# Optimization experiments

Measured on AMD Instinct MI355X. Metric: run time of the kernel, lower is better.

The kernel has to match this reference:

```python
import jax, jax.numpy as jnp
import numpy as np

N, E, F, H = 50000, 800000, 64, 4
NEG_SLOPE = 0.2
LN_EPS = 1e-5


def setup_inputs() -> dict:
    key = jax.random.key(0)
    ks = jax.random.split(key, 12)
    h = jax.random.normal(ks[0], (N, F), dtype=jnp.float32)
    src = jax.random.randint(ks[1], (E,), 0, N, dtype=jnp.int32)
    dst = jax.random.randint(ks[2], (E,), 0, N, dtype=jnp.int32)
    s = 1.0 / np.sqrt(F)
    fc_w = jax.random.uniform(ks[3], (F, H * F), jnp.float32, -s, s)
    attn_l = jax.random.normal(ks[4], (H, F), dtype=jnp.float32) * s
    attn_r = jax.random.normal(ks[5], (H, F), dtype=jnp.float32) * s
    gat_bias = jnp.zeros((H * F,), dtype=jnp.float32)
    so = 1.0 / np.sqrt(H * F)
    out_w = jax.random.uniform(ks[6], (H * F, F), jnp.float32, -so, so)
    out_b = jax.random.uniform(ks[7], (F,), jnp.float32, -so, so)
    ln_g = jnp.ones((F,), dtype=jnp.float32)
    ln_b = jnp.zeros((F,), dtype=jnp.float32)
    return {"h": h, "src": src, "dst": dst, "fc_w": fc_w, "attn_l": attn_l,
            "attn_r": attn_r, "gat_bias": gat_bias, "out_w": out_w,
            "out_b": out_b, "ln_g": ln_g, "ln_b": ln_b}


def reference(h, src, dst, fc_w, attn_l, attn_r, gat_bias, out_w, out_b, ln_g, ln_b):
    # --- GATConv (DGL semantics) ---
    feat = (h @ fc_w).reshape(N, H, F)                      # [N,H,F]
    el = jnp.einsum('nhf,hf->nh', feat, attn_l)             # [N,H]
    er = jnp.einsum('nhf,hf->nh', feat, attn_r)             # [N,H]
    e = jax.nn.leaky_relu(el[src] + er[dst], NEG_SLOPE)     # [E,H]
    # edge softmax over incoming edges of each dst node
    m = jax.ops.segment_max(e, dst, num_segments=N)         # [N,H]
    ex = jnp.exp(e - m[dst])                                # [E,H]
    z = jax.ops.segment_sum(ex, dst, num_segments=N)        # [N,H]
    alpha = ex / z[dst]                                     # [E,H]
    msg = feat[src] * alpha[:, :, None]                     # [E,H,F]
    rst = jax.ops.segment_sum(msg, dst, num_segments=N)     # [N,H,F]
    rst = rst + gat_bias.reshape(H, F)
    # --- out linear + layernorm ---
    x = rst.reshape(N, H * F) @ out_w + out_b               # [N,F]
    mu = jnp.mean(x, axis=-1, keepdims=True)
    var = jnp.var(x, axis=-1, keepdims=True)
    return (x - mu) * jax.lax.rsqrt(var + LN_EPS) * ln_g + ln_b
```

## Files before the change

### kernel.cpp

```cpp
#include <hip/hip_runtime.h>

#define NN 50000
#define EE 800000
#define FF 64
#define HH 4
#define HF 256
#define NEG_SLOPE 0.2f
#define LN_EPS 1e-5f
#define WPACK_N (4 * 8 * 64 * 8)
#define NTILE (NN / 16)
#define TROW 264

typedef __attribute__((ext_vector_type(8))) short s8v;
typedef __attribute__((ext_vector_type(4))) float f4v;

__device__ __forceinline__ unsigned short f32_to_bf16_rne(float x) {
  unsigned int u = __float_as_uint(x);
  unsigned int r = u + 0x7FFFu + ((u >> 16) & 1u);
  return (unsigned short)(r >> 16);
}

__device__ __forceinline__ float readlane_f(float v, int l) {
  return __uint_as_float(
      (unsigned)__builtin_amdgcn_readlane((int)__float_as_uint(v), l));
}

__global__ __launch_bounds__(256) void k_prep(
    const float* __restrict__ fc_w, const float* __restrict__ out_w,
    const float* __restrict__ attn_l, const float* __restrict__ attn_r,
    const float* __restrict__ gat_bias, const float* __restrict__ out_b,
    unsigned short* __restrict__ wpack, float* __restrict__ alv,
    float* __restrict__ arv, float* __restrict__ outb2,
    int* __restrict__ cnt) {
  const int idx = blockIdx.x * 256 + threadIdx.x;
  if (idx < WPACK_N) {
    const int j = idx & 7;
    const int l = (idx >> 3) & 63;
    const int t = (idx >> 9) & 7;
    const int ct = idx >> 12;
    const int k = 32 * t + (l >> 4) * 8 + j;
    const int c = 16 * ct + (l & 15);
    const int hh = k >> 6, kk = k & 63;
    const float* fw = fc_w + kk * HF + hh * FF;
    const float* ow = out_w + (size_t)(hh * FF) * FF + c;
    float acc = 0.f;
#pragma unroll
    for (int ff = 0; ff < FF; ++ff) acc = fmaf(fw[ff], ow[(size_t)ff * FF], acc);
    wpack[idx] = f32_to_bf16_rne(acc);
  } else if (idx < WPACK_N + 512) {
    const int i = idx - WPACK_N;
    const int hh = (i >> 6) & 3, kk = i & 63;
    const float* fw = fc_w + kk * HF + hh * FF;
    const float* at = (i < 256 ? attn_l : attn_r) + hh * FF;
    float acc = 0.f;
#pragma unroll
    for (int ff = 0; ff < FF; ++ff) acc = fmaf(fw[ff], at[ff], acc);
    (i < 256 ? alv : arv)[(hh << 6) | kk] = acc;
  } else if (idx < WPACK_N + 512 + FF) {
    const int c = idx - WPACK_N - 512;
    float acc = out_b[c];
    for (int k = 0; k < HF; ++k) acc = fmaf(gat_bias[k], out_w[(size_t)k * FF + c], acc);
    outb2[c] = acc;
  }
  if (idx < NN) cnt[idx] = 0;
}

__global__ __launch_bounds__(256) void k_elr(
    const float* __restrict__ h, const float* __restrict__ alv,
    const float* __restrict__ arv, unsigned short* __restrict__ hb,
    float* __restrict__ el, float* __restrict__ er) {
  const int wave = threadIdx.x >> 6;
  const int lane = threadIdx.x & 63;
  const int n0 = blockIdx.x * 16 + wave * 4;
  float av[4], bv[4];
#pragma unroll
  for (int hh = 0; hh < 4; ++hh) {
    av[hh] = alv[(hh << 6) | lane];
    bv[hh] = arv[(hh << 6) | lane];
  }
#pragma unroll
  for (int r = 0; r < 4; ++r) {
    const int n = n0 + r;
    const float hv = h[(size_t)n * FF + lane];
    hb[(size_t)n * FF + lane] = f32_to_bf16_rne(hv);
    float p[8];
#pragma unroll
    for (int hh = 0; hh < 4; ++hh) { p[hh] = hv * av[hh]; p[4 + hh] = hv * bv[hh]; }
#pragma unroll
    for (int off = 1; off < 64; off <<= 1) {
#pragma unroll
      for (int q = 0; q < 8; ++q) p[q] += __shfl_xor(p[q], off, 64);
    }
    if (lane == 0) {
      *(float4*)(el + (size_t)n * 4) = make_float4(p[0], p[1], p[2], p[3]);
      *(float4*)(er + (size_t)n * 4) = make_float4(p[4], p[5], p[6], p[7]);
    }
  }
}

__global__ void k_scatter(const int* __restrict__ src,
                          const int* __restrict__ dst,
                          int* __restrict__ cnt, int* __restrict__ colp) {
  int e = blockIdx.x * blockDim.x + threadIdx.x;
  if (e < EE) {
    const int d = dst[e];
    const int pos = atomicAdd(&cnt[d], 1);
    if (pos < 64) colp[(d << 6) | pos] = src[e];
  }
}

__global__ __launch_bounds__(256) void k_gather_out(
    const unsigned short* __restrict__ hb, const float* __restrict__ el,
    const float* __restrict__ er, const int* __restrict__ cnt,
    const int* __restrict__ colp,
    const unsigned short* __restrict__ wpack, const float* __restrict__ outb2,
    const float* __restrict__ ln_g, const float* __restrict__ ln_b,
    float* __restrict__ out) {
  __shared__ unsigned short tile[16][TROW];
  const int wave = threadIdx.x >> 6;
  const int lane = threadIdx.x & 63;
  const int n0 = blockIdx.x * 16;
  const unsigned short* fb = hb + lane;

#pragma unroll
  for (int r = 0; r < 4; ++r) {
    const int row = wave * 4 + r;
    const int n = n0 + row;
    const int m = cnt[n];
    const float4 erv = *(const float4*)(er + (size_t)n * 4);
    int s = 0;
    float w0 = 0.f, w1 = 0.f, w2 = 0.f, w3 = 0.f;
    if (lane < m) {
      s = colp[(n << 6) | lane];
      const float4 elv = *(const float4*)(el + (size_t)s * 4);
      float e0 = elv.x + erv.x, e1 = elv.y + erv.y;
      float e2 = elv.z + erv.z, e3 = elv.w + erv.w;
      e0 = e0 > 0.f ? e0 : NEG_SLOPE * e0;
      e1 = e1 > 0.f ? e1 : NEG_SLOPE * e1;
      e2 = e2 > 0.f ? e2 : NEG_SLOPE * e2;
      e3 = e3 > 0.f ? e3 : NEG_SLOPE * e3;
      w0 = __expf(e0); w1 = __expf(e1);
      w2 = __expf(e2); w3 = __expf(e3);
    }
    float z0 = w0, z1 = w1, z2 = w2, z3 = w3;
#pragma unroll
    for (int off = 1; off < 64; off <<= 1) {
      z0 += __shfl_xor(z0, off, 64);
      z1 += __shfl_xor(z1, off, 64);
      z2 += __shfl_xor(z2, off, 64);
      z3 += __shfl_xor(z3, off, 64);
    }
    w0 *= (z0 > 0.f ? 1.f / z0 : 0.f);
    w1 *= (z1 > 0.f ? 1.f / z1 : 0.f);
    w2 *= (z2 > 0.f ? 1.f / z2 : 0.f);
    w3 *= (z3 > 0.f ? 1.f / z3 : 0.f);

    float a0 = 0.f, a1 = 0.f, a2 = 0.f, a3 = 0.f;
    for (int e = 0; e < m; e += 8) {
#pragma unroll
      for (int j = 0; j < 8; ++j) {
        const int le = e + j;
        const int se = __builtin_amdgcn_readlane(s, le);
        const float xv = __uint_as_float(
            (unsigned)fb[(size_t)se * FF] << 16);
        const float we0 = readlane_f(w0, le);
        const float we1 = readlane_f(w1, le);
        const float we2 = readlane_f(w2, le);
        const float we3 = readlane_f(w3, le);
        a0 = fmaf(we0, xv, a0);
        a1 = fmaf(we1, xv, a1);
        a2 = fmaf(we2, xv, a2);
        a3 = fmaf(we3, xv, a3);
      }
    }
    tile[row][lane]       = f32_to_bf16_rne(a0);
    tile[row][64 + lane]  = f32_to_bf16_rne(a1);
    tile[row][128 + lane] = f32_to_bf16_rne(a2);
    tile[row][192 + lane] = f32_to_bf16_rne(a3);
  }
  __syncthreads();
  if (wave != 0) return;

  const int cl = lane & 15;
  const int quad = lane >> 4;
  s8v a[8];
#pragma unroll
  for (int t = 0; t < 8; ++t)
    a[t] = *(const s8v*)(&tile[cl][32 * t + quad * 8]);

  f4v acc[4];
#pragma unroll
  for (int ct = 0; ct < 4; ++ct) {
    f4v z = {0.f, 0.f, 0.f, 0.f};
    acc[ct] = z;
#pragma unroll
    for (int t = 0; t < 8; ++t) {
      const s8v b = *(const s8v*)(wpack + ((ct * 8 + t) * 64 + lane) * 8);
      acc[ct] = __builtin_amdgcn_mfma_f32_16x16x32_bf16(a[t], b, acc[ct], 0, 0, 0);
    }
  }

  float x[4][4];
  float s1[4], s2[4];
#pragma unroll
  for (int r = 0; r < 4; ++r) { s1[r] = 0.f; s2[r] = 0.f; }
#pragma unroll
  for (int ct = 0; ct < 4; ++ct) {
    const float ob = outb2[16 * ct + cl];
#pragma unroll
    for (int r = 0; r < 4; ++r) {
      const float v = acc[ct][r] + ob;
      x[ct][r] = v;
      s1[r] += v;
      s2[r] += v * v;
    }
  }
#pragma unroll
  for (int r = 0; r < 4; ++r) {
#pragma unroll
    for (int off = 1; off < 16; off <<= 1) {
      s1[r] += __shfl_xor(s1[r], off, 64);
      s2[r] += __shfl_xor(s2[r], off, 64);
    }
  }
#pragma unroll
  for (int r = 0; r < 4; ++r) {
    const float mu = s1[r] * (1.f / 64.f);
    const float var = s2[r] * (1.f / 64.f) - mu * mu;
    const float inv = rsqrtf(var + LN_EPS);
    const int row = n0 + quad * 4 + r;
#pragma unroll
    for (int ct = 0; ct < 4; ++ct) {
      const int c = 16 * ct + cl;
      out[(size_t)row * FF + c] = (x[ct][r] - mu) * inv * ln_g[c] + ln_b[c];
    }
  }
}

extern "C" void kernel_launch(void* const* d_in, const int* in_sizes, int n_in,
                              void* d_out, int out_size, void* d_ws,
                              size_t ws_size, hipStream_t stream) {
  const float* h_in   = (const float*)d_in[0];
  const int*   src    = (const int*)d_in[1];
  const int*   dst    = (const int*)d_in[2];
  const float* fc_w   = (const float*)d_in[3];
  const float* attn_l = (const float*)d_in[4];
  const float* attn_r = (const float*)d_in[5];
  const float* gbias  = (const float*)d_in[6];
  const float* out_w  = (const float*)d_in[7];
  const float* out_b  = (const float*)d_in[8];
  const float* ln_g   = (const float*)d_in[9];
  const float* ln_b   = (const float*)d_in[10];
  float* out = (float*)d_out;

  char* p = (char*)d_ws;
  auto alloc = [&](size_t bytes) {
    char* q = p;
    p += (bytes + 255) & ~(size_t)255;
    return q;
  };
  unsigned short* hb     = (unsigned short*)alloc((size_t)NN * FF * 2);
  unsigned short* wpack  = (unsigned short*)alloc((size_t)WPACK_N * 2);
  float* alv     = (float*)alloc(256 * 4);
  float* arv     = (float*)alloc(256 * 4);
  float* outb2   = (float*)alloc(64 * 4);
  float* el      = (float*)alloc((size_t)NN * HH * 4);
  float* er      = (float*)alloc((size_t)NN * HH * 4);
  int*   cnt     = (int*)alloc((size_t)NN * 4);
  int*   colp    = (int*)alloc((size_t)NN * 64 * 4);

  k_prep<<<256, 256, 0, stream>>>(fc_w, out_w, attn_l, attn_r, gbias, out_b,
                                  wpack, alv, arv, outb2, cnt);
  k_elr<<<NTILE, 256, 0, stream>>>(h_in, alv, arv, hb, el, er);
  k_scatter<<<(EE + 255) / 256, 256, 0, stream>>>(src, dst, cnt, colp);
  k_gather_out<<<NTILE, 256, 0, stream>>>(hb, el, er, cnt, colp, wpack,
                                          outb2, ln_g, ln_b, out);
}
```

Measured before the change: 217.9 us.

## Partition edge-bucket counters per XCD and store 16-bit source indices

The scatter kernel reads the hardware XCC id and keeps a separate counter and bucket array per XCD. Its atomics use relaxed ordering at workgroup scope, so they no longer contend with other XCDs on the same counter. Source indices are stored as 16-bit values with a per-partition cap of 48. The gather kernel merges the 8 partitions per node into a lane-indexed neighbor list. The cost is zeroing 8x as many counters in the prep kernel, 8 count loads per node, and bucket reads spread over a much larger buffer.

```diff
diff --git a/kernel.cpp b/kernel.cpp
--- a/kernel.cpp
+++ b/kernel.cpp
@@ -10,6 +10,8 @@
 #define WPACK_N (4 * 8 * 64 * 8)
 #define NTILE (NN / 16)
 #define TROW 264
+#define NXCD 8
+#define RCAP 48
 
 typedef __attribute__((ext_vector_type(8))) short s8v;
 typedef __attribute__((ext_vector_type(4))) float f4v;
@@ -31,7 +33,7 @@
     const float* __restrict__ gat_bias, const float* __restrict__ out_b,
     unsigned short* __restrict__ wpack, float* __restrict__ alv,
     float* __restrict__ arv, float* __restrict__ outb2,
-    int* __restrict__ cnt) {
+    int* __restrict__ cnt8) {
   const int idx = blockIdx.x * 256 + threadIdx.x;
   if (idx < WPACK_N) {
     const int j = idx & 7;
@@ -62,7 +64,7 @@
     for (int k = 0; k < HF; ++k) acc = fmaf(gat_bias[k], out_w[(size_t)k * FF + c], acc);
     outb2[c] = acc;
   }
-  if (idx < NN) cnt[idx] = 0;
+  if (idx < NXCD * NN) cnt8[idx] = 0;
 }
 
 __global__ __launch_bounds__(256) void k_elr(
@@ -98,21 +100,28 @@
   }
 }
 
-__global__ void k_scatter(const int* __restrict__ src,
-                          const int* __restrict__ dst,
-                          int* __restrict__ cnt, int* __restrict__ colp) {
-  int e = blockIdx.x * blockDim.x + threadIdx.x;
+__global__ __launch_bounds__(256) void k_scatter(
+    const int* __restrict__ src, const int* __restrict__ dst,
+    int* __restrict__ cnt8, unsigned short* __restrict__ colp8) {
+  unsigned xcd;
+  asm("s_getreg_b32 %0, hwreg(HW_REG_XCC_ID)" : "=s"(xcd));
+  xcd &= 7;
+  const int e = blockIdx.x * 256 + threadIdx.x;
   if (e < EE) {
     const int d = dst[e];
-    const int pos = atomicAdd(&cnt[d], 1);
-    if (pos < 64) colp[(d << 6) | pos] = src[e];
+    const int sv = src[e];
+    const int pos = __hip_atomic_fetch_add(&cnt8[xcd * NN + d], 1,
+                                           __ATOMIC_RELAXED,
+                                           __HIP_MEMORY_SCOPE_WORKGROUP);
+    if (pos < RCAP)
+      colp8[((size_t)xcd * NN + d) * RCAP + pos] = (unsigned short)sv;
   }
 }
 
 __global__ __launch_bounds__(256) void k_gather_out(
     const unsigned short* __restrict__ hb, const float* __restrict__ el,
-    const float* __restrict__ er, const int* __restrict__ cnt,
-    const int* __restrict__ colp,
+    const float* __restrict__ er, const int* __restrict__ cnt8,
+    const unsigned short* __restrict__ colp8,
     const unsigned short* __restrict__ wpack, const float* __restrict__ outb2,
     const float* __restrict__ ln_g, const float* __restrict__ ln_b,
     float* __restrict__ out) {
@@ -126,12 +135,23 @@
   for (int r = 0; r < 4; ++r) {
     const int row = wave * 4 + r;
     const int n = n0 + row;
-    const int m = cnt[n];
     const float4 erv = *(const float4*)(er + (size_t)n * 4);
-    int s = 0;
+
+    int px = 0, sel = 0;
+#pragma unroll
+    for (int x = 0; x < NXCD; ++x) {
+      int c = cnt8[x * NN + n];
+      c = c > RCAP ? RCAP : c;
+      const int rel = lane - px;
+      if (rel >= 0 && rel < c)
+        sel = colp8[((size_t)x * NN + n) * RCAP + rel];
+      px += c;
+    }
+    const int m = __builtin_amdgcn_readfirstlane(px > 64 ? 64 : px);
+    const int s = sel;
+
     float w0 = 0.f, w1 = 0.f, w2 = 0.f, w3 = 0.f;
     if (lane < m) {
-      s = colp[(n << 6) | lane];
       const float4 elv = *(const float4*)(el + (size_t)s * 4);
       float e0 = elv.x + erv.x, e1 = elv.y + erv.y;
       float e2 = elv.z + erv.z, e3 = elv.w + erv.w;
@@ -266,13 +286,14 @@
   float* outb2   = (float*)alloc(64 * 4);
   float* el      = (float*)alloc((size_t)NN * HH * 4);
   float* er      = (float*)alloc((size_t)NN * HH * 4);
-  int*   cnt     = (int*)alloc((size_t)NN * 4);
-  int*   colp    = (int*)alloc((size_t)NN * 64 * 4);
-
-  k_prep<<<256, 256, 0, stream>>>(fc_w, out_w, attn_l, attn_r, gbias, out_b,
-                                  wpack, alv, arv, outb2, cnt);
+  int*   cnt8    = (int*)alloc((size_t)NXCD * NN * 4);
+  unsigned short* colp8 =
+      (unsigned short*)alloc((size_t)NXCD * NN * RCAP * 2);
+
+  k_prep<<<(NXCD * NN + 255) / 256, 256, 0, stream>>>(
+      fc_w, out_w, attn_l, attn_r, gbias, out_b, wpack, alv, arv, outb2, cnt8);
   k_elr<<<NTILE, 256, 0, stream>>>(h_in, alv, arv, hb, el, er);
-  k_scatter<<<(EE + 255) / 256, 256, 0, stream>>>(src, dst, cnt, colp);
-  k_gather_out<<<NTILE, 256, 0, stream>>>(hb, el, er, cnt, colp, wpack,
+  k_scatter<<<(EE + 255) / 256, 256, 0, stream>>>(src, dst, cnt8, colp8);
+  k_gather_out<<<NTILE, 256, 0, stream>>>(hb, el, er, cnt8, colp8, wpack,
                                           outb2, ln_g, ln_b, out);
 }
```

New measurement: 227.5 us. +4.4%, slower.
